# Performance work log

Hardware: AMD Instinct MI355X
Metric: run time of the kernel (lower is better)

## Reference

```python
import jax, jax.numpy as jnp
import numpy as np

NQ = 8
DIM = 2 ** NQ  # 256 amplitudes
HALF_PI = float(np.pi / 2)

CNOT_M = jnp.array([[1, 0, 0, 0], [0, 1, 0, 0], [0, 0, 0, 1], [0, 0, 1, 0]], dtype=jnp.complex64)
SWAP_M = jnp.array([[1, 0, 0, 0], [0, 0, 1, 0], [0, 1, 0, 0], [0, 0, 0, 1]], dtype=jnp.complex64)

# PauliZ sign vectors per wire; wire 0 is the most-significant bit (PennyLane convention)
_bits = (np.arange(DIM)[None, :] >> (NQ - 1 - np.arange(NQ))[:, None]) & 1
ZSIGNS = jnp.asarray(1.0 - 2.0 * _bits, dtype=jnp.float32)  # [NQ, DIM]


def _rx(t):
    c = jnp.cos(0.5 * t).astype(jnp.complex64)
    s = (-1j * jnp.sin(0.5 * t)).astype(jnp.complex64)
    return jnp.stack([jnp.stack([c, s]), jnp.stack([s, c])])


def _ry(t):
    c = jnp.cos(0.5 * t).astype(jnp.complex64)
    s = jnp.sin(0.5 * t).astype(jnp.complex64)
    return jnp.stack([jnp.stack([c, -s]), jnp.stack([s, c])])


def _rz(t):
    e0 = jnp.exp(-0.5j * t).astype(jnp.complex64)
    e1 = jnp.exp(0.5j * t).astype(jnp.complex64)
    z = jnp.zeros((), jnp.complex64)
    return jnp.stack([jnp.stack([e0, z]), jnp.stack([z, e1])])


def _ixx(t):
    c = jnp.cos(0.5 * t).astype(jnp.complex64)
    s = (-1j * jnp.sin(0.5 * t)).astype(jnp.complex64)
    z = jnp.zeros((), jnp.complex64)
    return jnp.stack([jnp.stack([c, z, z, s]), jnp.stack([z, c, s, z]),
                      jnp.stack([z, s, c, z]), jnp.stack([s, z, z, c])])


def _apply_1q(psi, U, w):
    # psi: [B] + [2]*NQ ; apply 2x2 U on wire w
    psi = jnp.moveaxis(psi, 1 + w, -1)
    psi = psi @ U.T
    return jnp.moveaxis(psi, -1, 1 + w)


def _apply_2q(psi, U, w1, w2):
    # apply 4x4 U on wires (w1, w2); w1 is the more-significant wire of U
    psi = jnp.moveaxis(psi, (1 + w1, 1 + w2), (-2, -1))
    shp = psi.shape
    psi = (psi.reshape(shp[:-2] + (4,)) @ U.T).reshape(shp)
    return jnp.moveaxis(psi, (-2, -1), (1 + w1, 1 + w2))


def _edges_from_coupling(coupling):
    # Mirrors the torch code: threshold min-max normalized coupling at 0.5.
    # This is a non-differentiable, data-dependent circuit-structure decision,
    # so it is resolved on concrete values (as the Python ifs do in torch).
    c = np.asarray(jax.device_get(coupling), dtype=np.float64)
    cn = (c - c.min()) / (c.max() - c.min())
    adj = cn > 0.5
    return [(i, j) for i in range(NQ) for j in range(i + 1, NQ) if adj[i, j]]


def _conv(psi, i, j, p):
    psi = _apply_1q(psi, _rz(jnp.float32(-HALF_PI)), j)
    psi = _apply_2q(psi, CNOT_M, j, i)  # CNOT control=j target=i
    psi = _apply_1q(psi, _rz(p[0]), i)
    psi = _apply_1q(psi, _ry(p[1]), j)
    psi = _apply_2q(psi, CNOT_M, i, j)
    psi = _apply_1q(psi, _ry(p[2]), j)
    psi = _apply_2q(psi, CNOT_M, j, i)
    psi = _apply_1q(psi, _rz(jnp.float32(HALF_PI)), i)
    return psi


def _pool(psi, i, j, p):
    psi = _apply_1q(psi, _rz(jnp.float32(-HALF_PI)), j)
    psi = _apply_2q(psi, CNOT_M, j, i)
    psi = _apply_1q(psi, _rz(p[0]), i)
    psi = _apply_1q(psi, _ry(p[1]), j)
    psi = _apply_2q(psi, CNOT_M, i, j)
    psi = _apply_1q(psi, _ry(p[2]), j)
    return psi


def _circuit(x, weights, coupling, edges):
    B = x.shape[0]
    # AmplitudeEmbedding(normalize=True)
    psi = (x / jnp.linalg.norm(x, axis=1, keepdims=True)).astype(jnp.complex64)
    psi = psi.reshape((B,) + (2,) * NQ)
    for i in range(NQ):
        psi = _apply_1q(psi, _rx(weights[i]), i)
        psi = _apply_1q(psi, _ry(weights[i + NQ]), i)
        psi = _apply_1q(psi, _rz(weights[i + 2 * NQ]), i)
    for i in range(NQ):
        for j in range(i + 1, NQ):
            psi = _apply_2q(psi, _ixx(coupling[i, j]), i, j)
    widx = 3 * NQ
    for (i, j) in edges:
        nonadjacent = abs(i - j) != 1
        if nonadjacent:
            psi = _apply_2q(psi, SWAP_M, i, j)
        psi = _conv(psi, i, j, weights[widx:widx + 3])
        psi = _pool(psi, i, j, weights[widx + 3:widx + 6])
        widx += 6
        if nonadjacent:
            psi = _apply_2q(psi, SWAP_M, i, j)
    psi_f = psi.reshape(B, DIM)
    probs = psi_f.real ** 2 + psi_f.imag ** 2  # [B, DIM]
    return probs @ ZSIGNS.T  # [B, NQ] expval(PauliZ(i))


def setup_inputs() -> dict:
    B = 65536
    key = jax.random.key(0)
    k1, k2, k3 = jax.random.split(key, 3)
    x = jax.random.normal(k1, (B, DIM), dtype=jnp.float32)
    weights = jax.random.normal(k2, (3 * NQ + 6 * 28,), dtype=jnp.float32)  # 192: max edges = C(8,2)=28
    coupling = jax.random.normal(k3, (NQ, NQ), dtype=jnp.float32)
    return {"x": x, "weights": weights, "coupling": coupling}


def reference(x, weights, coupling):
    edges = _edges_from_coupling(coupling)
    return _circuit(x, weights, coupling, edges)
```

## Files before the change

kernel.cpp:

```cpp
#include <hip/hip_runtime.h>

#define HP 1.57079632679489662f

typedef float f32x4 __attribute__((ext_vector_type(4)));
typedef short sh4 __attribute__((ext_vector_type(4)));
typedef __bf16 bf16x8 __attribute__((ext_vector_type(8)));

__device__ __forceinline__ unsigned short f2bf(float f) {
  unsigned int u = __builtin_bit_cast(unsigned int, f);
  u += 0x7fffu + ((u >> 16) & 1u);
  return (unsigned short)(u >> 16);
}

__device__ __forceinline__ void rowswap4(float (&mr)[4][4], float (&mi)[4][4], int a, int b) {
#pragma unroll
  for (int c = 0; c < 4; c++) {
    float tr = mr[a][c]; mr[a][c] = mr[b][c]; mr[b][c] = tr;
    float ti = mi[a][c]; mi[a][c] = mi[b][c]; mi[b][c] = ti;
  }
}

__device__ __forceinline__ void absorb_rz(float (&mr)[4][4], float (&mi)[4][4], float t, int bitpos) {
  float ch = cosf(0.5f * t), sh = sinf(0.5f * t);
#pragma unroll
  for (int r = 0; r < 4; r++) {
    float ph = ((r >> bitpos) & 1) ? sh : -sh;
#pragma unroll
    for (int c = 0; c < 4; c++) {
      float ar = mr[r][c], ai = mi[r][c];
      mr[r][c] = ch * ar - ph * ai;
      mi[r][c] = ch * ai + ph * ar;
    }
  }
}

__device__ __forceinline__ void absorb_ry(float (&mr)[4][4], float (&mi)[4][4], float t, int bitpos) {
  float ch = cosf(0.5f * t), sh = sinf(0.5f * t);
#pragma unroll
  for (int r = 0; r < 4; r++) {
    if ((r >> bitpos) & 1) continue;
    int rb = r | (1 << bitpos);
#pragma unroll
    for (int c = 0; c < 4; c++) {
      float ar = mr[r][c], ai = mi[r][c];
      float br = mr[rb][c], bi = mi[rb][c];
      mr[r][c]  = ch * ar - sh * br;  mi[r][c]  = ch * ai - sh * bi;
      mr[rb][c] = sh * ar + ch * br;  mi[rb][c] = sh * ai + ch * bi;
    }
  }
}


__global__ __launch_bounds__(64) void build_u_wave(const float* __restrict__ wt,
                                                   const float* __restrict__ coup,
                                                   void* __restrict__ wsv) {
  unsigned char* Ub = (unsigned char*)wsv + 4096;
  const int c = blockIdx.x;
  const int lane = threadIdx.x;

  __shared__ float Q1s[64];
  __shared__ float E4s[28 * 32];
  __shared__ int metas[57];

  {
    double mn = 1e300, mx = -1e300;
    for (int k = 0; k < 64; k++) {
      double v = (double)coup[k];
      mn = v < mn ? v : mn;
      mx = v > mx ? v : mx;
    }
    int cnt = 0, myi = -1, myj = -1;
    for (int i = 0; i < 8; i++)
      for (int j = i + 1; j < 8; j++) {
        double cn = ((double)coup[i * 8 + j] - mn) / (mx - mn);
        if (cn > 0.5) {
          if (cnt == lane) { myi = i; myj = j; }
          cnt++;
        }
      }
    if (lane == 0) metas[0] = cnt;

    if (lane < 8) {
      float tx = wt[lane], ty = wt[8 + lane], tz = wt[16 + lane];
      float cx = cosf(0.5f * tx), sx = sinf(0.5f * tx);
      float cy = cosf(0.5f * ty), sy = sinf(0.5f * ty);
      float cz = cosf(0.5f * tz), sz = sinf(0.5f * tz);
      float m00r = cy * cx,  m00i = sy * sx;
      float m01r = -sy * cx, m01i = -cy * sx;
      float m10r = sy * cx,  m10i = -cy * sx;
      float m11r = cy * cx,  m11i = -sy * sx;
      float* q = Q1s + lane * 8;
      q[0] = cz * m00r + sz * m00i; q[1] = cz * m00i - sz * m00r;
      q[2] = cz * m01r + sz * m01i; q[3] = cz * m01i - sz * m01r;
      q[4] = cz * m10r - sz * m10i; q[5] = cz * m10i + sz * m10r;
      q[6] = cz * m11r - sz * m11i; q[7] = cz * m11i + sz * m11r;
    }

    if (lane < cnt && lane < 28) {
      float mr[4][4], mi[4][4];
#pragma unroll
      for (int r = 0; r < 4; r++)
#pragma unroll
        for (int cc = 0; cc < 4; cc++) { mr[r][cc] = (r == cc) ? 1.f : 0.f; mi[r][cc] = 0.f; }

      bool nonadj = (myj - myi) != 1;
      int wb = 24 + 6 * lane;

      if (nonadj) rowswap4(mr, mi, 1, 2);
      absorb_rz(mr, mi, -HP, 0);
      rowswap4(mr, mi, 1, 3);
      absorb_rz(mr, mi, wt[wb + 0], 1);
      absorb_ry(mr, mi, wt[wb + 1], 0);
      rowswap4(mr, mi, 2, 3);
      absorb_ry(mr, mi, wt[wb + 2], 0);
      rowswap4(mr, mi, 1, 3);
      absorb_rz(mr, mi, HP, 1);
      absorb_rz(mr, mi, -HP, 0);
      rowswap4(mr, mi, 1, 3);
      absorb_rz(mr, mi, wt[wb + 3], 1);
      absorb_ry(mr, mi, wt[wb + 4], 0);
      rowswap4(mr, mi, 2, 3);
      absorb_ry(mr, mi, wt[wb + 5], 0);
      if (nonadj) rowswap4(mr, mi, 1, 2);

      float* e = E4s + lane * 32;
#pragma unroll
      for (int r = 0; r < 4; r++)
#pragma unroll
        for (int cc = 0; cc < 4; cc++) {
          e[(r * 4 + cc) * 2]     = mr[r][cc];
          e[(r * 4 + cc) * 2 + 1] = mi[r][cc];
        }
      metas[1 + 2 * lane] = myi;
      metas[2 + 2 * lane] = myj;
    }
  }
  __syncthreads();

  float2 st[4];
#pragma unroll
  for (int q = 0; q < 4; q++)
    st[q] = make_float2((q * 64 + lane) == c ? 1.f : 0.f, 0.f);

  auto partner = [&](int M, float2 (&par)[4]) {
    const int qm = M >> 6, lm = M & 63;
    float2 t0, t1, t2, t3;
    if (qm == 0)      { t0 = st[0]; t1 = st[1]; t2 = st[2]; t3 = st[3]; }
    else if (qm == 1) { t0 = st[1]; t1 = st[0]; t2 = st[3]; t3 = st[2]; }
    else if (qm == 2) { t0 = st[2]; t1 = st[3]; t2 = st[0]; t3 = st[1]; }
    else              { t0 = st[3]; t1 = st[2]; t2 = st[1]; t3 = st[0]; }
    if (lm) {
      t0.x = __shfl_xor(t0.x, lm); t0.y = __shfl_xor(t0.y, lm);
      t1.x = __shfl_xor(t1.x, lm); t1.y = __shfl_xor(t1.y, lm);
      t2.x = __shfl_xor(t2.x, lm); t2.y = __shfl_xor(t2.y, lm);
      t3.x = __shfl_xor(t3.x, lm); t3.y = __shfl_xor(t3.y, lm);
    }
    par[0] = t0; par[1] = t1; par[2] = t2; par[3] = t3;
  };

  for (int wi = 0; wi < 8; wi++) {
    const float* M = Q1s + wi * 8;
    const int p = 7 - wi;
    float2 par[4];
    partner(1 << p, par);
    float m00r = M[0], m00i = M[1], m01r = M[2], m01i = M[3];
    float m10r = M[4], m10i = M[5], m11r = M[6], m11i = M[7];
#pragma unroll
    for (int q = 0; q < 4; q++) {
      int b = ((q * 64 + lane) >> p) & 1;
      float2 own = st[q], pr = par[q];
      float2 x0 = b ? pr : own;
      float2 x1 = b ? own : pr;
      float c0r = b ? m10r : m00r, c0i = b ? m10i : m00i;
      float c1r = b ? m11r : m01r, c1i = b ? m11i : m01i;
      st[q].x = c0r * x0.x - c0i * x0.y + c1r * x1.x - c1i * x1.y;
      st[q].y = c0r * x0.y + c0i * x0.x + c1r * x1.y + c1i * x1.x;
    }
  }

  for (int i = 0; i < 8; i++)
    for (int j = i + 1; j < 8; j++) {
      float t = coup[i * 8 + j];
      float ch = cosf(0.5f * t), sn = sinf(0.5f * t);
      int mask = (1 << (7 - i)) | (1 << (7 - j));
      float2 par[4];
      partner(mask, par);
#pragma unroll
      for (int q = 0; q < 4; q++) {
        float2 own = st[q], pr = par[q];
        st[q] = make_float2(ch * own.x + sn * pr.y, ch * own.y - sn * pr.x);
      }
    }

  int ne = metas[0];
  for (int e = 0; e < ne; e++) {
    int i = metas[1 + 2 * e], j = metas[2 + 2 * e];
    int p1 = 7 - i, p2 = 7 - j;
    int m1 = 1 << p1, m2 = 1 << p2;
    float2 pa2[4], pa1[4], pa12[4];
    partner(m2, pa2);
    partner(m1, pa1);
    partner(m1 | m2, pa12);
    const float* E = E4s + e * 32;
#pragma unroll
    for (int q = 0; q < 4; q++) {
      int r = q * 64 + lane;
      int b = ((r >> p1) & 1) * 2 + ((r >> p2) & 1);
      float nr = 0.f, ni = 0.f;
      { float Mr = E[(b * 4 + b) * 2], Mi = E[(b * 4 + b) * 2 + 1];
        nr += Mr * st[q].x - Mi * st[q].y; ni += Mr * st[q].y + Mi * st[q].x; }
      { int t2 = b ^ 1; float Mr = E[(b * 4 + t2) * 2], Mi = E[(b * 4 + t2) * 2 + 1];
        nr += Mr * pa2[q].x - Mi * pa2[q].y; ni += Mr * pa2[q].y + Mi * pa2[q].x; }
      { int t2 = b ^ 2; float Mr = E[(b * 4 + t2) * 2], Mi = E[(b * 4 + t2) * 2 + 1];
        nr += Mr * pa1[q].x - Mi * pa1[q].y; ni += Mr * pa1[q].y + Mi * pa1[q].x; }
      { int t2 = b ^ 3; float Mr = E[(b * 4 + t2) * 2], Mi = E[(b * 4 + t2) * 2 + 1];
        nr += Mr * pa12[q].x - Mi * pa12[q].y; ni += Mr * pa12[q].y + Mi * pa12[q].x; }
      st[q] = make_float2(nr, ni);
    }
  }

  {
    int ks = c >> 5, kc = c & 31;
    int sb = (kc >> 4) & 1, lg2 = (kc >> 2) & 3, ii = kc & 3;
#pragma unroll
    for (int q = 0; q < 4; q++) {
      int r = q * 64 + lane;
      int p = (lg2 + r) & 3;
      unsigned char* base = Ub + (size_t)ks * 32768 + (size_t)(2 * r) * 64 + p * 16 + sb * 8 + ii * 2;
      *(unsigned short*)(base)      = f2bf(st[q].x);
      *(unsigned short*)(base + 64) = f2bf(st[q].y);
    }
  }
}

#define MFMA_STEP(KS, AREG)                                                              \
  {                                                                                      \
    uint4 bq[4];                                                                         \
    _Pragma("unroll")                                                                    \
    for (int nf = 0; nf < 4; nf++) {                                                     \
      const int n = nf * 16 + lm;                                                        \
      int byte = (n * 512 + (KS) * 64 + lg * 16) ^ ((n & 7) << 4);                       \
      bq[nf] = *reinterpret_cast<const uint4*>(&smem[byte]);                             \
    }                                                                                    \
    __builtin_amdgcn_s_setprio(1);                                                       \
    _Pragma("unroll")                                                                    \
    for (int mf = 0; mf < 4; mf++) {                                                     \
      const sh4 alo = __builtin_bit_cast(sh4, make_uint2(AREG[mf].x, AREG[mf].y));       \
      const sh4 ahi = __builtin_bit_cast(sh4, make_uint2(AREG[mf].z, AREG[mf].w));       \
      _Pragma("unroll")                                                                  \
      for (int nf = 0; nf < 4; nf++) {                                                   \
        const sh4 blo = __builtin_bit_cast(sh4, make_uint2(bq[nf].x, bq[nf].y));         \
        const sh4 bhi = __builtin_bit_cast(sh4, make_uint2(bq[nf].z, bq[nf].w));         \
        acc[mf][nf] = __builtin_amdgcn_mfma_f32_16x16x16bf16_1k(alo, blo, acc[mf][nf], 0, 0, 0); \
        acc[mf][nf] = __builtin_amdgcn_mfma_f32_16x16x16bf16_1k(ahi, bhi, acc[mf][nf], 0, 0, 0); \
      }                                                                                  \
    }                                                                                    \
    __builtin_amdgcn_s_setprio(0);                                                       \
  }

__global__ __launch_bounds__(512, 4) void gemm_l2(const float* __restrict__ x,
                                                  const void* __restrict__ wsv,
                                                  float* __restrict__ out) {
  const unsigned char* Ub = (const unsigned char*)wsv + 4096;
  __shared__ __align__(16) unsigned char smem[32768];

  const int tid = threadIdx.x;
  const int tile = blockIdx.x;
  const int wv = tid >> 6;
  const int lane = tid & 63;
  const int lm = lane & 15;
  const int lg = lane >> 4;
  const int rot = (blockIdx.x >> 3) & 7;

  const unsigned char* abase[4];
#pragma unroll
  for (int mf = 0; mf < 4; mf++) {
    const int m = wv * 64 + mf * 16 + lm;
    const int p = (lg + (m >> 1)) & 3;
    abase[mf] = Ub + (size_t)m * 64 + p * 16;
  }
  uint4 aP[4], aQ[4];
#pragma unroll
  for (int mf = 0; mf < 4; mf++)
    aP[mf] = *reinterpret_cast<const uint4*>(abase[mf] + (size_t)rot * 32768);

  {
    const int rl = tid >> 3;
    const int seg = tid & 7;
    const float4* xs = (const float4*)(x + (size_t)(tile * 64 + rl) * 256 + seg * 32);
    float4 v[8];
    float ss = 0.f;
#pragma unroll
    for (int i = 0; i < 8; i++) {
      v[i] = xs[i];
      ss += v[i].x * v[i].x + v[i].y * v[i].y + v[i].z * v[i].z + v[i].w * v[i].w;
    }
    ss += __shfl_xor(ss, 1);
    ss += __shfl_xor(ss, 2);
    ss += __shfl_xor(ss, 4);
    float inv = 1.0f / sqrtf(ss);
    const float* vf = (const float*)v;
#pragma unroll
    for (int u = 0; u < 4; u++) {
      bf16x8 w;
#pragma unroll
      for (int j = 0; j < 8; j++)
        w[j] = (__bf16)(vf[16 * (j >> 2) + 4 * u + (j & 3)] * inv);
      uint4 pack = __builtin_bit_cast(uint4, w);
      int byte = (rl * 512 + seg * 64 + u * 16) ^ ((rl & 7) << 4);
      *reinterpret_cast<uint4*>(&smem[byte]) = pack;
    }
  }

  f32x4 acc[4][4] = {};
  __syncthreads();

#pragma unroll
  for (int kk = 0; kk < 4; kk++) {
    const int c0 = (2 * kk + rot) & 7;
    const int c1 = (2 * kk + 1 + rot) & 7;
#pragma unroll
    for (int mf = 0; mf < 4; mf++)
      aQ[mf] = *reinterpret_cast<const uint4*>(abase[mf] + (size_t)c1 * 32768);
    MFMA_STEP(c0, aP);
    if (kk < 3) {
      const int c2 = (2 * kk + 2 + rot) & 7;
#pragma unroll
      for (int mf = 0; mf < 4; mf++)
        aP[mf] = *reinterpret_cast<const uint4*>(abase[mf] + (size_t)c2 * 32768);
    }
    MFMA_STEP(c1, aQ);
  }
  __syncthreads();

  float pq[4][8];
#pragma unroll
  for (int nf = 0; nf < 4; nf++) {
    float T = 0.f, S7 = 0.f, S4 = 0.f, S3 = 0.f;
#pragma unroll
    for (int mf = 0; mf < 4; mf++) {
      f32x4 a = acc[mf][nf];
      float p0 = a[0] * a[0] + a[1] * a[1];
      float p1 = a[2] * a[2] + a[3] * a[3];
      float sp = p0 + p1, d = p0 - p1;
      T += sp;
      S7 += d;
      S4 += (mf & 1) ? -sp : sp;
      S3 += (mf & 2) ? -sp : sp;
    }
    pq[nf][7] = S7;
    pq[nf][6] = (lg & 1) ? -T : T;
    pq[nf][5] = (lg & 2) ? -T : T;
    pq[nf][4] = S4;
    pq[nf][3] = S3;
    pq[nf][2] = (wv & 1) ? -T : T;
    pq[nf][1] = (wv & 2) ? -T : T;
    pq[nf][0] = (wv & 4) ? -T : T;
  }
#pragma unroll
  for (int nf = 0; nf < 4; nf++)
#pragma unroll
    for (int k = 0; k < 8; k++) {
      pq[nf][k] += __shfl_xor(pq[nf][k], 16);
      pq[nf][k] += __shfl_xor(pq[nf][k], 32);
    }

  float* part = (float*)smem;
  if (lg == 0) {
#pragma unroll
    for (int nf = 0; nf < 4; nf++) {
      float* dst = part + (wv * 64 + nf * 16 + lm) * 8;
#pragma unroll
      for (int k = 0; k < 8; k++) dst[k] = pq[nf][k];
    }
  }
  __syncthreads();
  {
    int b = tid >> 3, q = tid & 7;
    float v2 = 0.f;
#pragma unroll
    for (int w2 = 0; w2 < 8; w2++) v2 += part[(w2 * 64 + b) * 8 + q];
    out[(size_t)(tile * 64 + b) * 8 + q] = v2;
  }
}

extern "C" void kernel_launch(void* const* d_in, const int* in_sizes, int n_in,
                              void* d_out, int out_size, void* d_ws, size_t ws_size,
                              hipStream_t stream) {
  const float* x    = (const float*)d_in[0];
  const float* wt   = (const float*)d_in[1];
  const float* coup = (const float*)d_in[2];
  float* out = (float*)d_out;

  build_u_wave<<<256, 64, 0, stream>>>(wt, coup, d_ws);
  gemm_l2<<<1024, 512, 0, stream>>>(x, d_ws, out);
}
```

Before: 70.69 us.

## Process two tiles per GEMM block with x prefetch and LDS-based unitary build

The GEMM kernel now handles two 64-row tiles per block, 512 blocks instead of 1024. It prefetches the second tile's x rows into registers while the first tile's MFMAs run, and reloads the first A fragment early. LDS per block doubles to 64KB and launch bounds drop to 2 blocks per CU, and the per-block rotation of the K-chunk order is removed. The unitary-build kernel also switches from register shuffles to a shared-memory state vector for gate application, trading shuffle traffic for LDS reads.

```diff
diff --git a/kernel.cpp b/kernel.cpp
--- a/kernel.cpp
+++ b/kernel.cpp
@@ -58,6 +58,7 @@
   const int c = blockIdx.x;
   const int lane = threadIdx.x;
 
+  __shared__ float2 s[256];
   __shared__ float Q1s[64];
   __shared__ float E4s[28 * 32];
   __shared__ int metas[57];
@@ -135,47 +136,27 @@
       metas[2 + 2 * lane] = myj;
     }
   }
-  __syncthreads();
-
-  float2 st[4];
+
 #pragma unroll
   for (int q = 0; q < 4; q++)
-    st[q] = make_float2((q * 64 + lane) == c ? 1.f : 0.f, 0.f);
-
-  auto partner = [&](int M, float2 (&par)[4]) {
-    const int qm = M >> 6, lm = M & 63;
-    float2 t0, t1, t2, t3;
-    if (qm == 0)      { t0 = st[0]; t1 = st[1]; t2 = st[2]; t3 = st[3]; }
-    else if (qm == 1) { t0 = st[1]; t1 = st[0]; t2 = st[3]; t3 = st[2]; }
-    else if (qm == 2) { t0 = st[2]; t1 = st[3]; t2 = st[0]; t3 = st[1]; }
-    else              { t0 = st[3]; t1 = st[2]; t2 = st[1]; t3 = st[0]; }
-    if (lm) {
-      t0.x = __shfl_xor(t0.x, lm); t0.y = __shfl_xor(t0.y, lm);
-      t1.x = __shfl_xor(t1.x, lm); t1.y = __shfl_xor(t1.y, lm);
-      t2.x = __shfl_xor(t2.x, lm); t2.y = __shfl_xor(t2.y, lm);
-      t3.x = __shfl_xor(t3.x, lm); t3.y = __shfl_xor(t3.y, lm);
-    }
-    par[0] = t0; par[1] = t1; par[2] = t2; par[3] = t3;
-  };
+    s[q * 64 + lane] = make_float2((q * 64 + lane) == c ? 1.f : 0.f, 0.f);
 
   for (int wi = 0; wi < 8; wi++) {
-    const float* M = Q1s + wi * 8;
     const int p = 7 - wi;
-    float2 par[4];
-    partner(1 << p, par);
-    float m00r = M[0], m00i = M[1], m01r = M[2], m01i = M[3];
-    float m10r = M[4], m10i = M[5], m11r = M[6], m11i = M[7];
+    const int m = 1 << p;
+    float2 nw[4];
 #pragma unroll
     for (int q = 0; q < 4; q++) {
-      int b = ((q * 64 + lane) >> p) & 1;
-      float2 own = st[q], pr = par[q];
-      float2 x0 = b ? pr : own;
-      float2 x1 = b ? own : pr;
-      float c0r = b ? m10r : m00r, c0i = b ? m10i : m00i;
-      float c1r = b ? m11r : m01r, c1i = b ? m11i : m01i;
-      st[q].x = c0r * x0.x - c0i * x0.y + c1r * x1.x - c1i * x1.y;
-      st[q].y = c0r * x0.y + c0i * x0.x + c1r * x1.y + c1i * x1.x;
-    }
+      int r = q * 64 + lane;
+      int b = (r >> p) & 1;
+      float2 a0 = s[r & ~m];
+      float2 a1 = s[r | m];
+      float4 Mv = *reinterpret_cast<const float4*>(&Q1s[wi * 8 + b * 4]);
+      nw[q].x = Mv.x * a0.x - Mv.y * a0.y + Mv.z * a1.x - Mv.w * a1.y;
+      nw[q].y = Mv.x * a0.y + Mv.y * a0.x + Mv.z * a1.y + Mv.w * a1.x;
+    }
+#pragma unroll
+    for (int q = 0; q < 4; q++) s[q * 64 + lane] = nw[q];
   }
 
   for (int i = 0; i < 8; i++)
@@ -183,13 +164,16 @@
       float t = coup[i * 8 + j];
       float ch = cosf(0.5f * t), sn = sinf(0.5f * t);
       int mask = (1 << (7 - i)) | (1 << (7 - j));
-      float2 par[4];
-      partner(mask, par);
+      float2 nw[4];
 #pragma unroll
       for (int q = 0; q < 4; q++) {
-        float2 own = st[q], pr = par[q];
-        st[q] = make_float2(ch * own.x + sn * pr.y, ch * own.y - sn * pr.x);
-      }
+        int r = q * 64 + lane;
+        float2 own = s[r];
+        float2 pr = s[r ^ mask];
+        nw[q] = make_float2(ch * own.x + sn * pr.y, ch * own.y - sn * pr.x);
+      }
+#pragma unroll
+      for (int q = 0; q < 4; q++) s[q * 64 + lane] = nw[q];
     }
 
   int ne = metas[0];
@@ -197,26 +181,25 @@
     int i = metas[1 + 2 * e], j = metas[2 + 2 * e];
     int p1 = 7 - i, p2 = 7 - j;
     int m1 = 1 << p1, m2 = 1 << p2;
-    float2 pa2[4], pa1[4], pa12[4];
-    partner(m2, pa2);
-    partner(m1, pa1);
-    partner(m1 | m2, pa12);
-    const float* E = E4s + e * 32;
+    float2 nw[4];
 #pragma unroll
     for (int q = 0; q < 4; q++) {
       int r = q * 64 + lane;
       int b = ((r >> p1) & 1) * 2 + ((r >> p2) & 1);
-      float nr = 0.f, ni = 0.f;
-      { float Mr = E[(b * 4 + b) * 2], Mi = E[(b * 4 + b) * 2 + 1];
-        nr += Mr * st[q].x - Mi * st[q].y; ni += Mr * st[q].y + Mi * st[q].x; }
-      { int t2 = b ^ 1; float Mr = E[(b * 4 + t2) * 2], Mi = E[(b * 4 + t2) * 2 + 1];
-        nr += Mr * pa2[q].x - Mi * pa2[q].y; ni += Mr * pa2[q].y + Mi * pa2[q].x; }
-      { int t2 = b ^ 2; float Mr = E[(b * 4 + t2) * 2], Mi = E[(b * 4 + t2) * 2 + 1];
-        nr += Mr * pa1[q].x - Mi * pa1[q].y; ni += Mr * pa1[q].y + Mi * pa1[q].x; }
-      { int t2 = b ^ 3; float Mr = E[(b * 4 + t2) * 2], Mi = E[(b * 4 + t2) * 2 + 1];
-        nr += Mr * pa12[q].x - Mi * pa12[q].y; ni += Mr * pa12[q].y + Mi * pa12[q].x; }
-      st[q] = make_float2(nr, ni);
-    }
+      int base = r & ~(m1 | m2);
+      float2 a0 = s[base];
+      float2 a1 = s[base | m2];
+      float2 a2 = s[base | m1];
+      float2 a3 = s[base | m1 | m2];
+      float4 M01 = *reinterpret_cast<const float4*>(&E4s[e * 32 + b * 8]);
+      float4 M23 = *reinterpret_cast<const float4*>(&E4s[e * 32 + b * 8 + 4]);
+      nw[q].x = M01.x * a0.x - M01.y * a0.y + M01.z * a1.x - M01.w * a1.y
+              + M23.x * a2.x - M23.y * a2.y + M23.z * a3.x - M23.w * a3.y;
+      nw[q].y = M01.x * a0.y + M01.y * a0.x + M01.z * a1.y + M01.w * a1.x
+              + M23.x * a2.y + M23.y * a2.x + M23.z * a3.y + M23.w * a3.x;
+    }
+#pragma unroll
+    for (int q = 0; q < 4; q++) s[q * 64 + lane] = nw[q];
   }
 
   {
@@ -227,19 +210,20 @@
       int r = q * 64 + lane;
       int p = (lg2 + r) & 3;
       unsigned char* base = Ub + (size_t)ks * 32768 + (size_t)(2 * r) * 64 + p * 16 + sb * 8 + ii * 2;
-      *(unsigned short*)(base)      = f2bf(st[q].x);
-      *(unsigned short*)(base + 64) = f2bf(st[q].y);
-    }
-  }
-}
-
-#define MFMA_STEP(KS, AREG)                                                              \
+      float2 a = s[r];
+      *(unsigned short*)(base)      = f2bf(a.x);
+      *(unsigned short*)(base + 64) = f2bf(a.y);
+    }
+  }
+}
+
+#define MFMA_STEP(PSIOFF, KS, AREG)                                                      \
   {                                                                                      \
     uint4 bq[4];                                                                         \
     _Pragma("unroll")                                                                    \
     for (int nf = 0; nf < 4; nf++) {                                                     \
       const int n = nf * 16 + lm;                                                        \
-      int byte = (n * 512 + (KS) * 64 + lg * 16) ^ ((n & 7) << 4);                       \
+      int byte = (PSIOFF) + ((n * 512 + (KS) * 64 + lg * 16) ^ ((n & 7) << 4));          \
       bq[nf] = *reinterpret_cast<const uint4*>(&smem[byte]);                             \
     }                                                                                    \
     __builtin_amdgcn_s_setprio(1);                                                       \
@@ -258,19 +242,20 @@
     __builtin_amdgcn_s_setprio(0);                                                       \
   }
 
-__global__ __launch_bounds__(512, 4) void gemm_l2(const float* __restrict__ x,
-                                                  const void* __restrict__ wsv,
-                                                  float* __restrict__ out) {
+__global__ __launch_bounds__(512, 2) void gemm_pipe(const float* __restrict__ x,
+                                                    const void* __restrict__ wsv,
+                                                    float* __restrict__ out) {
   const unsigned char* Ub = (const unsigned char*)wsv + 4096;
-  __shared__ __align__(16) unsigned char smem[32768];
+  __shared__ __align__(16) unsigned char smem[65536];
 
   const int tid = threadIdx.x;
-  const int tile = blockIdx.x;
+  const int bid = blockIdx.x;
   const int wv = tid >> 6;
   const int lane = tid & 63;
   const int lm = lane & 15;
   const int lg = lane >> 4;
-  const int rot = (blockIdx.x >> 3) & 7;
+  const int rl = tid >> 3;
+  const int seg = tid & 7;
 
   const unsigned char* abase[4];
 #pragma unroll
@@ -281,106 +266,122 @@
   }
   uint4 aP[4], aQ[4];
 #pragma unroll
-  for (int mf = 0; mf < 4; mf++)
-    aP[mf] = *reinterpret_cast<const uint4*>(abase[mf] + (size_t)rot * 32768);
-
+  for (int mf = 0; mf < 4; mf++) aP[mf] = *reinterpret_cast<const uint4*>(abase[mf]);
+
+  float4 vbuf[8];
   {
-    const int rl = tid >> 3;
-    const int seg = tid & 7;
-    const float4* xs = (const float4*)(x + (size_t)(tile * 64 + rl) * 256 + seg * 32);
-    float4 v[8];
-    float ss = 0.f;
-#pragma unroll
-    for (int i = 0; i < 8; i++) {
-      v[i] = xs[i];
-      ss += v[i].x * v[i].x + v[i].y * v[i].y + v[i].z * v[i].z + v[i].w * v[i].w;
-    }
-    ss += __shfl_xor(ss, 1);
-    ss += __shfl_xor(ss, 2);
-    ss += __shfl_xor(ss, 4);
-    float inv = 1.0f / sqrtf(ss);
-    const float* vf = (const float*)v;
-#pragma unroll
-    for (int u = 0; u < 4; u++) {
-      bf16x8 w;
-#pragma unroll
-      for (int j = 0; j < 8; j++)
-        w[j] = (__bf16)(vf[16 * (j >> 2) + 4 * u + (j & 3)] * inv);
-      uint4 pack = __builtin_bit_cast(uint4, w);
-      int byte = (rl * 512 + seg * 64 + u * 16) ^ ((rl & 7) << 4);
-      *reinterpret_cast<uint4*>(&smem[byte]) = pack;
-    }
-  }
-
-  f32x4 acc[4][4] = {};
-  __syncthreads();
-
-#pragma unroll
-  for (int kk = 0; kk < 4; kk++) {
-    const int c0 = (2 * kk + rot) & 7;
-    const int c1 = (2 * kk + 1 + rot) & 7;
-#pragma unroll
-    for (int mf = 0; mf < 4; mf++)
-      aQ[mf] = *reinterpret_cast<const uint4*>(abase[mf] + (size_t)c1 * 32768);
-    MFMA_STEP(c0, aP);
-    if (kk < 3) {
-      const int c2 = (2 * kk + 2 + rot) & 7;
+    const float4* xs = (const float4*)(x + (size_t)(bid * 2 * 64 + rl) * 256 + seg * 32);
+#pragma unroll
+    for (int i = 0; i < 8; i++) vbuf[i] = xs[i];
+  }
+
+  for (int t = 0; t < 2; t++) {
+    const int tile = bid * 2 + t;
+    const int psioff = t * 32768;
+
+    {
+      float ss = 0.f;
+#pragma unroll
+      for (int i = 0; i < 8; i++)
+        ss += vbuf[i].x * vbuf[i].x + vbuf[i].y * vbuf[i].y + vbuf[i].z * vbuf[i].z + vbuf[i].w * vbuf[i].w;
+      ss += __shfl_xor(ss, 1);
+      ss += __shfl_xor(ss, 2);
+      ss += __shfl_xor(ss, 4);
+      float inv = 1.0f / sqrtf(ss);
+      const float* vf = (const float*)vbuf;
+#pragma unroll
+      for (int u = 0; u < 4; u++) {
+        bf16x8 w;
+#pragma unroll
+        for (int j = 0; j < 8; j++)
+          w[j] = (__bf16)(vf[16 * (j >> 2) + 4 * u + (j & 3)] * inv);
+        uint4 pack = __builtin_bit_cast(uint4, w);
+        int byte = psioff + ((rl * 512 + seg * 64 + u * 16) ^ ((rl & 7) << 4));
+        *reinterpret_cast<uint4*>(&smem[byte]) = pack;
+      }
+    }
+
+    if (t == 0) {
+      const float4* xs1 = (const float4*)(x + (size_t)((bid * 2 + 1) * 64 + rl) * 256 + seg * 32);
+#pragma unroll
+      for (int i = 0; i < 8; i++) vbuf[i] = xs1[i];
+    }
+
+    f32x4 acc[4][4] = {};
+    __syncthreads();
+
+#pragma unroll
+    for (int kk = 0; kk < 4; kk++) {
 #pragma unroll
       for (int mf = 0; mf < 4; mf++)
-        aP[mf] = *reinterpret_cast<const uint4*>(abase[mf] + (size_t)c2 * 32768);
-    }
-    MFMA_STEP(c1, aQ);
-  }
-  __syncthreads();
-
-  float pq[4][8];
-#pragma unroll
-  for (int nf = 0; nf < 4; nf++) {
-    float T = 0.f, S7 = 0.f, S4 = 0.f, S3 = 0.f;
-#pragma unroll
-    for (int mf = 0; mf < 4; mf++) {
-      f32x4 a = acc[mf][nf];
-      float p0 = a[0] * a[0] + a[1] * a[1];
-      float p1 = a[2] * a[2] + a[3] * a[3];
-      float sp = p0 + p1, d = p0 - p1;
-      T += sp;
-      S7 += d;
-      S4 += (mf & 1) ? -sp : sp;
-      S3 += (mf & 2) ? -sp : sp;
-    }
-    pq[nf][7] = S7;
-    pq[nf][6] = (lg & 1) ? -T : T;
-    pq[nf][5] = (lg & 2) ? -T : T;
-    pq[nf][4] = S4;
-    pq[nf][3] = S3;
-    pq[nf][2] = (wv & 1) ? -T : T;
-    pq[nf][1] = (wv & 2) ? -T : T;
-    pq[nf][0] = (wv & 4) ? -T : T;
-  }
-#pragma unroll
-  for (int nf = 0; nf < 4; nf++)
-#pragma unroll
-    for (int k = 0; k < 8; k++) {
-      pq[nf][k] += __shfl_xor(pq[nf][k], 16);
-      pq[nf][k] += __shfl_xor(pq[nf][k], 32);
-    }
-
-  float* part = (float*)smem;
-  if (lg == 0) {
-#pragma unroll
-    for (int nf = 0; nf < 4; nf++) {
-      float* dst = part + (wv * 64 + nf * 16 + lm) * 8;
-#pragma unroll
-      for (int k = 0; k < 8; k++) dst[k] = pq[nf][k];
-    }
-  }
-  __syncthreads();
-  {
-    int b = tid >> 3, q = tid & 7;
-    float v2 = 0.f;
-#pragma unroll
-    for (int w2 = 0; w2 < 8; w2++) v2 += part[(w2 * 64 + b) * 8 + q];
-    out[(size_t)(tile * 64 + b) * 8 + q] = v2;
+        aQ[mf] = *reinterpret_cast<const uint4*>(abase[mf] + (size_t)(2 * kk + 1) * 32768);
+      MFMA_STEP(psioff, 2 * kk, aP);
+      if (kk < 3) {
+#pragma unroll
+        for (int mf = 0; mf < 4; mf++)
+          aP[mf] = *reinterpret_cast<const uint4*>(abase[mf] + (size_t)(2 * kk + 2) * 32768);
+      }
+      MFMA_STEP(psioff, 2 * kk + 1, aQ);
+    }
+
+    if (t == 0) {
+#pragma unroll
+      for (int mf = 0; mf < 4; mf++) aP[mf] = *reinterpret_cast<const uint4*>(abase[mf]);
+    }
+    __syncthreads();
+
+    {
+      float pq[4][8];
+#pragma unroll
+      for (int nf = 0; nf < 4; nf++) {
+        float T = 0.f, S7 = 0.f, S4 = 0.f, S3 = 0.f;
+#pragma unroll
+        for (int mf = 0; mf < 4; mf++) {
+          f32x4 a = acc[mf][nf];
+          float p0 = a[0] * a[0] + a[1] * a[1];
+          float p1 = a[2] * a[2] + a[3] * a[3];
+          float sp = p0 + p1, d = p0 - p1;
+          T += sp;
+          S7 += d;
+          S4 += (mf & 1) ? -sp : sp;
+          S3 += (mf & 2) ? -sp : sp;
+        }
+        pq[nf][7] = S7;
+        pq[nf][6] = (lg & 1) ? -T : T;
+        pq[nf][5] = (lg & 2) ? -T : T;
+        pq[nf][4] = S4;
+        pq[nf][3] = S3;
+        pq[nf][2] = (wv & 1) ? -T : T;
+        pq[nf][1] = (wv & 2) ? -T : T;
+        pq[nf][0] = (wv & 4) ? -T : T;
+      }
+#pragma unroll
+      for (int nf = 0; nf < 4; nf++)
+#pragma unroll
+        for (int k = 0; k < 8; k++) {
+          pq[nf][k] += __shfl_xor(pq[nf][k], 16);
+          pq[nf][k] += __shfl_xor(pq[nf][k], 32);
+        }
+
+      float* part = (float*)smem;
+      if (lg == 0) {
+#pragma unroll
+        for (int nf = 0; nf < 4; nf++) {
+          float* dst = part + (wv * 64 + nf * 16 + lm) * 8;
+#pragma unroll
+          for (int k = 0; k < 8; k++) dst[k] = pq[nf][k];
+        }
+      }
+      __syncthreads();
+      {
+        int b = tid >> 3, q = tid & 7;
+        float v2 = 0.f;
+#pragma unroll
+        for (int w2 = 0; w2 < 8; w2++) v2 += part[(w2 * 64 + b) * 8 + q];
+        out[(size_t)(tile * 64 + b) * 8 + q] = v2;
+      }
+      __syncthreads();
+    }
   }
 }
 
@@ -393,5 +394,5 @@
   float* out = (float*)d_out;
 
   build_u_wave<<<256, 64, 0, stream>>>(wt, coup, d_ws);
-  gemm_l2<<<1024, 512, 0, stream>>>(x, d_ws, out);
-}
+  gemm_pipe<<<512, 512, 0, stream>>>(x, d_ws, out);
+}
```

New measurement: 97.97 us. 38.6% more time.
